# Kernel optimization log

Measured on AMD Instinct MI355X. Metric: run time of the kernel, lower is better.

The kernel has to match this reference:

```python
import jax, jax.numpy as jnp
import numpy as np

IN_C, HEAD_C, EXPAND_C, OUT_C, TIME_C, H = 512, 64, 2048, 512, 256, 8
EPS = 1e-5

def _layernorm(x, g, b):
    mu = jnp.mean(x, axis=-1, keepdims=True)
    var = jnp.mean((x - mu) ** 2, axis=-1, keepdims=True)
    return (x - mu) * jax.lax.rsqrt(var + EPS) * g + b

def setup_inputs() -> dict:
    key = jax.random.key(0)
    ks = jax.random.split(key, 12)
    B, N = 4, 2048
    qkv_dim = HEAD_C * H * 2 + IN_C * H
    def lin(k, fan_in, fan_out):
        bound = 1.0 / np.sqrt(fan_in)
        kw, kb = jax.random.split(k)
        W = jax.random.uniform(kw, (fan_in, fan_out), jnp.float32, -bound, bound)
        b = jax.random.uniform(kb, (fan_out,), jnp.float32, -bound, bound)
        return W, b
    qkv_w, qkv_b = lin(ks[0], IN_C, qkv_dim)
    merge_w, merge_b = lin(ks[1], IN_C * H, IN_C)
    time_w, time_b = lin(ks[2], TIME_C, TIME_C)
    ff1_w, ff1_b = lin(ks[3], IN_C + TIME_C, EXPAND_C)
    ff2_w, ff2_b = lin(ks[4], EXPAND_C, OUT_C)
    return {
        'x': jax.random.normal(ks[5], (B, N, IN_C), jnp.float32),
        't': jax.random.normal(ks[6], (B, TIME_C), jnp.float32),
        'ln1_g': jnp.ones((IN_C,), jnp.float32), 'ln1_b': jnp.zeros((IN_C,), jnp.float32),
        'qkv_w': qkv_w, 'qkv_b': qkv_b,
        'merge_w': merge_w, 'merge_b': merge_b,
        'time_w': time_w, 'time_b': time_b,
        'ln2_g': jnp.ones((IN_C + TIME_C,), jnp.float32), 'ln2_b': jnp.zeros((IN_C + TIME_C,), jnp.float32),
        'ff1_w': ff1_w, 'ff1_b': ff1_b,
        'ff2_w': ff2_w, 'ff2_b': ff2_b,
    }

def reference(x, t, ln1_g, ln1_b, qkv_w, qkv_b, merge_w, merge_b,
              time_w, time_b, ln2_g, ln2_b, ff1_w, ff1_b, ff2_w, ff2_b):
    B, N, _ = x.shape
    scale = HEAD_C ** -0.5
    qkv = _layernorm(x, ln1_g, ln1_b) @ qkv_w + qkv_b
    q, k, v = jnp.split(qkv, [HEAD_C * H, 2 * HEAD_C * H], axis=-1)
    q = q.reshape(B, N, H, HEAD_C)          # B N H Cq
    k = k.reshape(B, N, H, HEAD_C)
    v = v.reshape(B, N, H, IN_C)            # V per head has dim in_c (as in source)
    attn = jnp.einsum('bnhc,bmhc->bhnm', q, k) * scale
    attn = jax.nn.softmax(attn, axis=-1)    # dropout = identity (eval)
    out = jnp.einsum('bhnm,bmhd->bnhd', attn, v).reshape(B, N, H * IN_C)
    x = x + out @ merge_w + merge_b
    tt = (t @ time_w + time_b)[:, None, :]  # B 1 time_c, broadcasts over N
    tt = jnp.broadcast_to(tt, (B, N, TIME_C))
    h = _layernorm(jnp.concatenate([x, tt], axis=-1), ln2_g, ln2_b)
    h = jax.nn.gelu(h @ ff1_w + ff1_b, approximate=False)
    return x + (h @ ff2_w + ff2_b)          # shortcut = Identity (in_c == out_c)
```

## Files before the change

kernel.cpp:

```cpp
#include <hip/hip_runtime.h>

#define IN_C 512
#define HEAD_C 64
#define NHEAD 8
#define TIME_C 256
#define EXPAND_C 2048
#define NB 4
#define NN 2048
#define QKV_DIM 5120
#define ROWS (NB*NN)
#define MERGE_K (NHEAD*IN_C)
#define LN2_C (IN_C+TIME_C)

typedef __bf16 bf16x8 __attribute__((ext_vector_type(8)));
typedef float f32x4 __attribute__((ext_vector_type(4)));
typedef float f32x16 __attribute__((ext_vector_type(16)));
typedef unsigned int u32x4 __attribute__((ext_vector_type(4)));

__device__ __forceinline__ unsigned short f2bf(float f){
  unsigned int u = __builtin_bit_cast(unsigned int, f);
  u += 0x7fffu + ((u >> 16) & 1u);
  return (unsigned short)(u >> 16);
}
__device__ __forceinline__ unsigned int cvtpk(float a, float b){
  unsigned int r;
  asm("v_cvt_pk_bf16_f32 %0, %1, %2" : "=v"(r) : "v"(a), "v"(b));
  return r;
}
__device__ __forceinline__ float vexp2(float x){
  float r;
  asm("v_exp_f32 %0, %1" : "=v"(r) : "v"(x));
  return r;
}
__device__ __forceinline__ float bpermf(float v, int srclane){
  int r = __builtin_amdgcn_ds_bpermute(srclane<<2, __builtin_bit_cast(int, v));
  return __builtin_bit_cast(float, r);
}
__device__ __forceinline__ void gload16(const unsigned short* g, unsigned short* l){
  __builtin_amdgcn_global_load_lds(
      (const __attribute__((address_space(1))) void*)g,
      (__attribute__((address_space(3))) void*)l, 16, 0, 0);
}

__global__ __launch_bounds__(256) void k_transpose_w(const float* __restrict__ W,
                                                     unsigned short* __restrict__ Wt,
                                                     int K, int N){
  __shared__ unsigned short tile[64*72];
  int t = threadIdx.x;
  int kb = blockIdx.y<<6, nb = blockIdx.x<<6;
  {
    int kr = t>>2, nc = (t&3)<<4;
    const float* src = W + (size_t)(kb+kr)*N + nb + nc;
    alignas(16) unsigned short tmp[16];
    #pragma unroll
    for (int j=0;j<16;j+=4){
      float4 v = *(const float4*)(src + j);
      tmp[j+0]=f2bf(v.x); tmp[j+1]=f2bf(v.y); tmp[j+2]=f2bf(v.z); tmp[j+3]=f2bf(v.w);
    }
    *(bf16x8*)&tile[kr*72 + nc]     = *(bf16x8*)&tmp[0];
    *(bf16x8*)&tile[kr*72 + nc + 8] = *(bf16x8*)&tmp[8];
  }
  __syncthreads();
  {
    int nr = t>>2, kc = (t&3)<<4;
    alignas(16) unsigned short ov[16];
    #pragma unroll
    for (int i=0;i<16;i++) ov[i] = tile[(kc+i)*72 + nr];
    unsigned short* dst = Wt + (size_t)(nb+nr)*K + kb + kc;
    *(bf16x8*)dst     = *(bf16x8*)&ov[0];
    *(bf16x8*)(dst+8) = *(bf16x8*)&ov[8];
  }
}

__global__ __launch_bounds__(256) void k_repack_k(const unsigned short* __restrict__ qkv,
                                                  unsigned short* __restrict__ Kf){
  __shared__ unsigned short tile[64*72];
  int j = blockIdx.x;
  int kb64 = j&31, bh = j>>5;
  int b = bh>>3, hh = bh&7;
  int t = threadIdx.x;
  {
    int key = t>>2, sc = t&3;
    const unsigned short* src = qkv + (size_t)(b*NN + kb64*64 + key)*QKV_DIM + IN_C + hh*HEAD_C;
    *(bf16x8*)&tile[key*72 + sc*8]     = *(const bf16x8*)(src + sc*8);
    *(bf16x8*)&tile[key*72 + (sc+4)*8] = *(const bf16x8*)(src + (sc+4)*8);
  }
  __syncthreads();
  int l = t&63, w = t>>6;
  int kb32l = w&1, kk0 = w>>1;
  #pragma unroll
  for (int i=0;i<2;i++){
    int kk = kk0 + i*2;
    alignas(16) unsigned short ov[8];
    #pragma unroll
    for (int jj=0;jj<8;jj++)
      ov[jj] = tile[(kb32l*32 + (l&31))*72 + kk*16 + (l>>5)*8 + jj];
    size_t dst = (((size_t)(bh*64 + kb64*2 + kb32l))*4 + kk)*512 + l*8;
    *(bf16x8*)(Kf + dst) = *(bf16x8*)ov;
  }
}

__global__ __launch_bounds__(256) void k_repack_v(const unsigned short* __restrict__ qkv,
                                                  unsigned short* __restrict__ Vf){
  __shared__ unsigned short tile[64*136];
  int j = blockIdx.x;
  int kb64 = j&31, bh = j>>5;
  int b = bh>>3, hh = bh&7;
  int t = threadIdx.x, l = t&63, w = t>>6;
  int key = t>>2, sc = t&3;
  const unsigned short* srow = qkv + (size_t)(b*NN + kb64*64 + key)*QKV_DIM + 2*IN_C + hh*IN_C;
  for (int p=0;p<4;p++){
    #pragma unroll
    for (int i=0;i<4;i++){
      int ch = sc + i*4;
      *(bf16x8*)&tile[key*136 + ch*8] = *(const bf16x8*)(srow + p*128 + ch*8);
    }
    __syncthreads();
    #pragma unroll
    for (int dbl=0;dbl<4;dbl++){
      alignas(16) unsigned short ov[8];
      #pragma unroll
      for (int jj=0;jj<8;jj++)
        ov[jj] = tile[(w*16 + (l>>5)*8 + jj)*136 + dbl*32 + (l&31)];
      size_t dst = (((size_t)(bh*128 + kb64*4 + w))*16 + p*4 + dbl)*512 + l*8;
      *(bf16x8*)(Vf + dst) = *(bf16x8*)ov;
    }
    __syncthreads();
  }
}

__global__ __launch_bounds__(256) void k_ln1(const float* __restrict__ x,
                                             const float* __restrict__ g,
                                             const float* __restrict__ bta,
                                             unsigned short* __restrict__ out){
  int row = (blockIdx.x<<2) + (threadIdx.x>>6);
  int l = threadIdx.x&63;
  const float* px = x + (size_t)row*IN_C + l*8;
  alignas(16) float v[8];
  *(float4*)&v[0] = *(const float4*)px;
  *(float4*)&v[4] = *(const float4*)(px+4);
  float s=0.f, sq=0.f;
  #pragma unroll
  for (int j=0;j<8;j++){ s+=v[j]; sq+=v[j]*v[j]; }
  #pragma unroll
  for (int d=32; d>0; d>>=1){ s += __shfl_xor(s,d); sq += __shfl_xor(sq,d); }
  float mu = s*(1.f/IN_C);
  float var = sq*(1.f/IN_C) - mu*mu;
  float rstd = rsqrtf(var + 1e-5f);
  alignas(16) unsigned short o[8];
  #pragma unroll
  for (int j=0;j<8;j++){
    int c = l*8+j;
    o[j] = f2bf((v[j]-mu)*rstd*g[c] + bta[c]);
  }
  *(bf16x8*)(out + (size_t)row*IN_C + l*8) = *(bf16x8*)o;
}

__global__ __launch_bounds__(256) void k_time(const float* __restrict__ t,
                                              const float* __restrict__ W,
                                              const float* __restrict__ bias,
                                              float* __restrict__ tt){
  int b = blockIdx.x, j = threadIdx.x;
  float acc = bias[j];
  const float* tr = t + b*TIME_C;
  #pragma unroll 4
  for (int c=0;c<TIME_C;c++) acc = fmaf(tr[c], W[c*TIME_C + j], acc);
  tt[b*TIME_C + j] = acc;
}

__global__ __launch_bounds__(256) void k_ln2(const float* __restrict__ x2,
                                             const float* __restrict__ tt,
                                             const float* __restrict__ g,
                                             const float* __restrict__ bta,
                                             unsigned short* __restrict__ out){
  int row = (blockIdx.x<<2) + (threadIdx.x>>6);
  int l = threadIdx.x&63;
  int bi = row>>11;
  float v[12];
  int c0 = l*12;
  #pragma unroll
  for (int j=0;j<12;j++){
    int c = c0+j;
    v[j] = (c < IN_C) ? x2[(size_t)row*IN_C + c] : tt[bi*TIME_C + c - IN_C];
  }
  float s=0.f, sq=0.f;
  #pragma unroll
  for (int j=0;j<12;j++){ s+=v[j]; sq+=v[j]*v[j]; }
  #pragma unroll
  for (int d=32; d>0; d>>=1){ s += __shfl_xor(s,d); sq += __shfl_xor(sq,d); }
  float mu = s*(1.f/LN2_C);
  float var = sq*(1.f/LN2_C) - mu*mu;
  float rstd = rsqrtf(var + 1e-5f);
  #pragma unroll
  for (int j=0;j<12;j++){
    int c = c0+j;
    out[(size_t)row*LN2_C + c] = f2bf((v[j]-mu)*rstd*g[c] + bta[c]);
  }
}

template<int EPI>
__global__ __launch_bounds__(256) void k_gemm(const unsigned short* __restrict__ A, int lda,
                                              const unsigned short* __restrict__ Bt, int ldb,
                                              const float* __restrict__ bias,
                                              const float* __restrict__ res, int ldres,
                                              void* __restrict__ Cp, int ldc, int K){
  __shared__ unsigned short sA[128*64];
  __shared__ unsigned short sB[128*64];
  int t = threadIdx.x;
  int l = t&63, w = t>>6;
  int m0 = blockIdx.y<<7, n0 = blockIdx.x<<7;
  int wr = (w>>1)<<6, wc = (w&1)<<6;
  int lm = l&15, kq = (l>>4)<<3;
  f32x4 acc[4][4] = {};
  int srow = l>>3, scol = (l&7)<<3;
  const unsigned short* pA = A + (size_t)m0*lda;
  const unsigned short* pB = Bt + (size_t)n0*ldb;
  for (int k0=0; k0<K; k0+=64){
    #pragma unroll
    for (int i=0;i<4;i++){
      int c = w*4 + i;
      gload16(pA + (size_t)(c*8 + srow)*lda + k0 + scol, &sA[c*512]);
      gload16(pB + (size_t)(c*8 + srow)*ldb + k0 + scol, &sB[c*512]);
    }
    __syncthreads();
    bf16x8 af[2][4], bfv[2][4];
    #pragma unroll
    for (int kk=0;kk<2;kk++)
      #pragma unroll
      for (int i=0;i<4;i++){
        af[kk][i]  = *(const bf16x8*)&sA[(wr + i*16 + lm)*64 + kk*32 + kq];
        bfv[kk][i] = *(const bf16x8*)&sB[(wc + i*16 + lm)*64 + kk*32 + kq];
      }
    #pragma unroll
    for (int kk=0;kk<2;kk++)
      #pragma unroll
      for (int mi=0;mi<4;mi++)
        #pragma unroll
        for (int ni=0;ni<4;ni++)
          acc[mi][ni] = __builtin_amdgcn_mfma_f32_16x16x32_bf16(af[kk][mi], bfv[kk][ni], acc[mi][ni], 0,0,0);
    __syncthreads();
  }
  int lr4 = (l>>4)<<2;
  #pragma unroll
  for (int mi=0;mi<4;mi++){
    int row0 = m0 + wr + mi*16 + lr4;
    #pragma unroll
    for (int ni=0;ni<4;ni++){
      int col = n0 + wc + ni*16 + lm;
      float bi = bias[col];
      #pragma unroll
      for (int r=0;r<4;r++){
        float v = acc[mi][ni][r] + bi;
        int row = row0 + r;
        if (EPI==1){
          v += res[(size_t)row*ldres + col];
          ((float*)Cp)[(size_t)row*ldc + col] = v;
        } else if (EPI==2){
          v = 0.5f*v*(1.f + erff(v*0.70710678118f));
          ((unsigned short*)Cp)[(size_t)row*ldc + col] = f2bf(v);
        } else {
          ((unsigned short*)Cp)[(size_t)row*ldc + col] = f2bf(v);
        }
      }
    }
  }
}

__global__ __launch_bounds__(256, 2) void k_attn(const unsigned short* __restrict__ qkv,
                                                 const unsigned short* __restrict__ Kf,
                                                 const unsigned short* __restrict__ Vf,
                                                 unsigned short* __restrict__ out){
  int j = blockIdx.x;
  int xcd = j&7;
  int rest = j>>3;
  int bh = xcd + ((rest>>6)<<3);
  int inner = rest&63;
  int qb = inner>>2, dh = inner&3;
  int b = bh>>3, hh = bh&7;
  int t = threadIdx.x, l = t&63, w = t>>6;
  int q0 = qb*128 + w*32;
  int lq = l&31, half = l>>5;

  bf16x8 qf[4];
  #pragma unroll
  for (int kk=0;kk<4;kk++)
    qf[kk] = *(const bf16x8*)(qkv + (size_t)(b*NN + q0 + lq)*QKV_DIM + hh*HEAD_C + kk*16 + half*8);

  f32x16 o[4] = {};
  float l_ = 0.f;

  const unsigned short* Kbase = Kf + (size_t)bh*64*2048 + l*8;
  const unsigned short* Vbase = Vf + ((size_t)bh*128*16 + dh*4)*512 + l*8;

  auto loadchunk = [&](int c, bf16x8 (&kfv)[4], bf16x8 (&vfv)[2][4]){
    const unsigned short* kp = Kbase + (size_t)c*2048;
    #pragma unroll
    for (int kk=0;kk<4;kk++)
      kfv[kk] = *(const bf16x8*)(kp + kk*512);
    const unsigned short* vp = Vbase + (size_t)c*16384;
    #pragma unroll
    for (int kc=0;kc<2;kc++)
      #pragma unroll
      for (int dn=0;dn<4;dn++)
        vfv[kc][dn] = *(const bf16x8*)(vp + kc*8192 + dn*512);
  };

  auto body = [&](bf16x8 (&kfv)[4], bf16x8 (&vfv)[2][4]){
    f32x16 s = {};
    s = __builtin_amdgcn_mfma_f32_32x32x16_bf16(kfv[0], qf[0], s, 0,0,0);
    s = __builtin_amdgcn_mfma_f32_32x32x16_bf16(kfv[1], qf[1], s, 0,0,0);
    s = __builtin_amdgcn_mfma_f32_32x32x16_bf16(kfv[2], qf[2], s, 0,0,0);
    s = __builtin_amdgcn_mfma_f32_32x32x16_bf16(kfv[3], qf[3], s, 0,0,0);

    float pv[16]; float ps = 0.f;
    #pragma unroll
    for (int r=0;r<16;r++){
      pv[r] = vexp2(s[r]*0.18033688f);
      ps += pv[r];
    }
    ps += __shfl_xor(ps, 32);
    l_ += ps;

    unsigned int wv[8], xw[8];
    #pragma unroll
    for (int jj=0;jj<8;jj++) wv[jj] = cvtpk(pv[2*jj], pv[2*jj+1]);
    #pragma unroll
    for (int jj=0;jj<8;jj++) xw[jj] = __shfl_xor(wv[jj], 32);
    u32x4 f0 = half ? (u32x4){xw[2],xw[3],wv[2],wv[3]} : (u32x4){wv[0],wv[1],xw[0],xw[1]};
    u32x4 f1 = half ? (u32x4){xw[6],xw[7],wv[6],wv[7]} : (u32x4){wv[4],wv[5],xw[4],xw[5]};
    bf16x8 pf0 = __builtin_bit_cast(bf16x8, f0);
    bf16x8 pf1 = __builtin_bit_cast(bf16x8, f1);

    #pragma unroll
    for (int dn=0;dn<4;dn++){
      o[dn] = __builtin_amdgcn_mfma_f32_32x32x16_bf16(pf0, vfv[0][dn], o[dn], 0,0,0);
      o[dn] = __builtin_amdgcn_mfma_f32_32x32x16_bf16(pf1, vfv[1][dn], o[dn], 0,0,0);
    }
  };

  bf16x8 kfa[4], vfa[2][4], kfb[4], vfb[2][4];
  loadchunk(0, kfa, vfa);
  for (int c=0; c<64; c+=2){
    loadchunk(c+1, kfb, vfb);
    body(kfa, vfa);
    if (c+2 < 64) loadchunk(c+2, kfa, vfa);
    body(kfb, vfb);
  }

  float invl = 1.f / l_;
  #pragma unroll
  for (int r=0;r<16;r++){
    int qr = (r&3) + 8*(r>>2) + 4*half;
    float il = bpermf(invl, qr);
    size_t row = (size_t)(b*NN + q0 + qr);
    #pragma unroll
    for (int dn=0;dn<4;dn++){
      int col = hh*IN_C + dh*128 + dn*32 + lq;
      out[row*MERGE_K + col] = f2bf(o[dn][r]*il);
    }
  }
}

extern "C" void kernel_launch(void* const* d_in, const int* in_sizes, int n_in,
                              void* d_out, int out_size, void* d_ws, size_t ws_size,
                              hipStream_t stream){
  const float* x       = (const float*)d_in[0];
  const float* tin     = (const float*)d_in[1];
  const float* ln1_g   = (const float*)d_in[2];
  const float* ln1_b   = (const float*)d_in[3];
  const float* qkv_w   = (const float*)d_in[4];
  const float* qkv_b   = (const float*)d_in[5];
  const float* merge_w = (const float*)d_in[6];
  const float* merge_b = (const float*)d_in[7];
  const float* time_w  = (const float*)d_in[8];
  const float* time_b  = (const float*)d_in[9];
  const float* ln2_g   = (const float*)d_in[10];
  const float* ln2_b   = (const float*)d_in[11];
  const float* ff1_w   = (const float*)d_in[12];
  const float* ff1_b   = (const float*)d_in[13];
  const float* ff2_w   = (const float*)d_in[14];
  const float* ff2_b   = (const float*)d_in[15];

  char* ws = (char*)d_ws;
  size_t off = 0;
  auto alloc = [&](size_t bytes)->void*{ void* p = ws + off; off += (bytes + 255) & ~(size_t)255; return p; };
  unsigned short* wqkvT   = (unsigned short*)alloc((size_t)QKV_DIM*IN_C*2);
  unsigned short* wmergeT = (unsigned short*)alloc((size_t)IN_C*MERGE_K*2);
  unsigned short* wff1T   = (unsigned short*)alloc((size_t)EXPAND_C*LN2_C*2);
  unsigned short* wff2T   = (unsigned short*)alloc((size_t)IN_C*EXPAND_C*2);
  float*          ttb     = (float*)alloc((size_t)NB*TIME_C*4);
  unsigned short* ln1o    = (unsigned short*)alloc((size_t)ROWS*IN_C*2);
  unsigned short* qkvb    = (unsigned short*)alloc((size_t)ROWS*QKV_DIM*2);
  unsigned short* kfrag   = (unsigned short*)alloc((size_t)32*64*4*64*8*2);
  unsigned short* vfrag   = (unsigned short*)alloc((size_t)32*128*16*64*8*2);
  unsigned short* atto    = (unsigned short*)alloc((size_t)ROWS*MERGE_K*2);
  float*          x2      = (float*)alloc((size_t)ROWS*IN_C*4);
  unsigned short* ln2o = vfrag;
  unsigned short* hbuf = qkvb;

  k_transpose_w<<<dim3(QKV_DIM/64, IN_C/64),  256, 0, stream>>>(qkv_w,   wqkvT,   IN_C,     QKV_DIM);
  k_transpose_w<<<dim3(IN_C/64,   MERGE_K/64),256, 0, stream>>>(merge_w, wmergeT, MERGE_K,  IN_C);
  k_transpose_w<<<dim3(EXPAND_C/64, LN2_C/64),256, 0, stream>>>(ff1_w,   wff1T,   LN2_C,    EXPAND_C);
  k_transpose_w<<<dim3(IN_C/64,   EXPAND_C/64),256, 0, stream>>>(ff2_w,  wff2T,   EXPAND_C, IN_C);
  k_time<<<dim3(NB), 256, 0, stream>>>(tin, time_w, time_b, ttb);
  k_ln1<<<dim3(ROWS/4), 256, 0, stream>>>(x, ln1_g, ln1_b, ln1o);

  k_gemm<0><<<dim3(QKV_DIM/128, ROWS/128), 256, 0, stream>>>(ln1o, IN_C, wqkvT, IN_C, qkv_b, nullptr, 0, qkvb, QKV_DIM, IN_C);
  k_repack_k<<<dim3(1024), 256, 0, stream>>>(qkvb, kfrag);
  k_repack_v<<<dim3(1024), 256, 0, stream>>>(qkvb, vfrag);
  k_attn<<<dim3(2048), 256, 0, stream>>>(qkvb, kfrag, vfrag, atto);
  k_gemm<1><<<dim3(IN_C/128, ROWS/128), 256, 0, stream>>>(atto, MERGE_K, wmergeT, MERGE_K, merge_b, x, IN_C, x2, IN_C, MERGE_K);
  k_ln2<<<dim3(ROWS/4), 256, 0, stream>>>(x2, ttb, ln2_g, ln2_b, ln2o);
  k_gemm<2><<<dim3(EXPAND_C/128, ROWS/128), 256, 0, stream>>>(ln2o, LN2_C, wff1T, LN2_C, ff1_b, nullptr, 0, hbuf, EXPAND_C, LN2_C);
  k_gemm<1><<<dim3(IN_C/128, ROWS/128), 256, 0, stream>>>(hbuf, EXPAND_C, wff2T, EXPAND_C, ff2_b, x2, IN_C, (float*)d_out, IN_C, EXPAND_C);

  (void)in_sizes; (void)n_in; (void)out_size; (void)ws_size;
}
```

Baseline: 645.4 us.

## Narrow N-tile for merge/ff2 GEMMs, simplify attention loop, vectorize LN2

Makes the GEMM N tile a template parameter and uses 64-wide tiles for the two GEMMs with output width 512, doubling their block count so the machine is better filled. The attention kernel folds the softmax scale into Q once, drops the per-chunk cross-lane sum in favor of one reduction at the end, and replaces manual double-buffered register prefetch with a simple loop under a higher occupancy bound (4 blocks/SM). LN2 uses float4 loads and 8-byte packed stores. Risks include less latency hiding in attention if the higher occupancy is not reached or causes spills, slight precision change from rounding the pre-scaled Q to bf16, and lower reuse in the narrower GEMM tiles.

```diff
diff --git a/kernel.cpp b/kernel.cpp
--- a/kernel.cpp
+++ b/kernel.cpp
@@ -16,6 +16,7 @@
 typedef float f32x4 __attribute__((ext_vector_type(4)));
 typedef float f32x16 __attribute__((ext_vector_type(16)));
 typedef unsigned int u32x4 __attribute__((ext_vector_type(4)));
+typedef unsigned short u16x4v __attribute__((ext_vector_type(4)));
 
 __device__ __forceinline__ unsigned short f2bf(float f){
   unsigned int u = __builtin_bit_cast(unsigned int, f);
@@ -176,12 +177,15 @@
   int row = (blockIdx.x<<2) + (threadIdx.x>>6);
   int l = threadIdx.x&63;
   int bi = row>>11;
-  float v[12];
   int c0 = l*12;
-  #pragma unroll
-  for (int j=0;j<12;j++){
-    int c = c0+j;
-    v[j] = (c < IN_C) ? x2[(size_t)row*IN_C + c] : tt[bi*TIME_C + c - IN_C];
+  alignas(16) float v[12], gg[12], bb[12];
+  #pragma unroll
+  for (int q=0;q<3;q++){
+    int c = c0 + q*4;
+    const float* src = (c < IN_C) ? &x2[(size_t)row*IN_C + c] : &tt[bi*TIME_C + c - IN_C];
+    *(float4*)&v[q*4]  = *(const float4*)src;
+    *(float4*)&gg[q*4] = *(const float4*)&g[c];
+    *(float4*)&bb[q*4] = *(const float4*)&bta[c];
   }
   float s=0.f, sq=0.f;
   #pragma unroll
@@ -191,27 +195,31 @@
   float mu = s*(1.f/LN2_C);
   float var = sq*(1.f/LN2_C) - mu*mu;
   float rstd = rsqrtf(var + 1e-5f);
-  #pragma unroll
-  for (int j=0;j<12;j++){
-    int c = c0+j;
-    out[(size_t)row*LN2_C + c] = f2bf((v[j]-mu)*rstd*g[c] + bta[c]);
-  }
-}
-
-template<int EPI>
+  alignas(8) unsigned short ov[12];
+  #pragma unroll
+  for (int j=0;j<12;j++)
+    ov[j] = f2bf((v[j]-mu)*rstd*gg[j] + bb[j]);
+  unsigned short* po = out + (size_t)row*LN2_C + c0;
+  *(u16x4v*)&po[0] = *(u16x4v*)&ov[0];
+  *(u16x4v*)&po[4] = *(u16x4v*)&ov[4];
+  *(u16x4v*)&po[8] = *(u16x4v*)&ov[8];
+}
+
+template<int EPI, int BN>
 __global__ __launch_bounds__(256) void k_gemm(const unsigned short* __restrict__ A, int lda,
                                               const unsigned short* __restrict__ Bt, int ldb,
                                               const float* __restrict__ bias,
                                               const float* __restrict__ res, int ldres,
                                               void* __restrict__ Cp, int ldc, int K){
+  constexpr int NI = BN/32;
   __shared__ unsigned short sA[128*64];
-  __shared__ unsigned short sB[128*64];
+  __shared__ unsigned short sB[BN*64];
   int t = threadIdx.x;
   int l = t&63, w = t>>6;
-  int m0 = blockIdx.y<<7, n0 = blockIdx.x<<7;
-  int wr = (w>>1)<<6, wc = (w&1)<<6;
+  int m0 = blockIdx.y<<7, n0 = blockIdx.x*BN;
+  int wr = (w>>1)<<6, wc = (w&1)*(BN/2);
   int lm = l&15, kq = (l>>4)<<3;
-  f32x4 acc[4][4] = {};
+  f32x4 acc[4][NI] = {};
   int srow = l>>3, scol = (l&7)<<3;
   const unsigned short* pA = A + (size_t)m0*lda;
   const unsigned short* pB = Bt + (size_t)n0*ldb;
@@ -220,23 +228,29 @@
     for (int i=0;i<4;i++){
       int c = w*4 + i;
       gload16(pA + (size_t)(c*8 + srow)*lda + k0 + scol, &sA[c*512]);
+    }
+    #pragma unroll
+    for (int i=0;i<BN/32;i++){
+      int c = w*(BN/32) + i;
       gload16(pB + (size_t)(c*8 + srow)*ldb + k0 + scol, &sB[c*512]);
     }
     __syncthreads();
-    bf16x8 af[2][4], bfv[2][4];
-    #pragma unroll
-    for (int kk=0;kk<2;kk++)
+    bf16x8 af[2][4], bfv[2][NI];
+    #pragma unroll
+    for (int kk=0;kk<2;kk++){
       #pragma unroll
-      for (int i=0;i<4;i++){
+      for (int i=0;i<4;i++)
         af[kk][i]  = *(const bf16x8*)&sA[(wr + i*16 + lm)*64 + kk*32 + kq];
+      #pragma unroll
+      for (int i=0;i<NI;i++)
         bfv[kk][i] = *(const bf16x8*)&sB[(wc + i*16 + lm)*64 + kk*32 + kq];
-      }
+    }
     #pragma unroll
     for (int kk=0;kk<2;kk++)
       #pragma unroll
       for (int mi=0;mi<4;mi++)
         #pragma unroll
-        for (int ni=0;ni<4;ni++)
+        for (int ni=0;ni<NI;ni++)
           acc[mi][ni] = __builtin_amdgcn_mfma_f32_16x16x32_bf16(af[kk][mi], bfv[kk][ni], acc[mi][ni], 0,0,0);
     __syncthreads();
   }
@@ -245,7 +259,7 @@
   for (int mi=0;mi<4;mi++){
     int row0 = m0 + wr + mi*16 + lr4;
     #pragma unroll
-    for (int ni=0;ni<4;ni++){
+    for (int ni=0;ni<NI;ni++){
       int col = n0 + wc + ni*16 + lm;
       float bi = bias[col];
       #pragma unroll
@@ -266,7 +280,7 @@
   }
 }
 
-__global__ __launch_bounds__(256, 2) void k_attn(const unsigned short* __restrict__ qkv,
+__global__ __launch_bounds__(256, 4) void k_attn(const unsigned short* __restrict__ qkv,
                                                  const unsigned short* __restrict__ Kf,
                                                  const unsigned short* __restrict__ Vf,
                                                  unsigned short* __restrict__ out){
@@ -283,8 +297,18 @@
 
   bf16x8 qf[4];
   #pragma unroll
-  for (int kk=0;kk<4;kk++)
-    qf[kk] = *(const bf16x8*)(qkv + (size_t)(b*NN + q0 + lq)*QKV_DIM + hh*HEAD_C + kk*16 + half*8);
+  for (int kk=0;kk<4;kk++){
+    bf16x8 raw = *(const bf16x8*)(qkv + (size_t)(b*NN + q0 + lq)*QKV_DIM + hh*HEAD_C + kk*16 + half*8);
+    u32x4 u = __builtin_bit_cast(u32x4, raw);
+    u32x4 rr;
+    #pragma unroll
+    for (int jj=0;jj<4;jj++){
+      float lo = __builtin_bit_cast(float, (u[jj]&0xffffu)<<16);
+      float hi = __builtin_bit_cast(float, u[jj]&0xffff0000u);
+      rr[jj] = cvtpk(lo*0.18033688f, hi*0.18033688f);
+    }
+    qf[kk] = __builtin_bit_cast(bf16x8, rr);
+  }
 
   f32x16 o[4] = {};
   float l_ = 0.f;
@@ -292,33 +316,25 @@
   const unsigned short* Kbase = Kf + (size_t)bh*64*2048 + l*8;
   const unsigned short* Vbase = Vf + ((size_t)bh*128*16 + dh*4)*512 + l*8;
 
-  auto loadchunk = [&](int c, bf16x8 (&kfv)[4], bf16x8 (&vfv)[2][4]){
+  for (int c=0;c<64;c++){
     const unsigned short* kp = Kbase + (size_t)c*2048;
-    #pragma unroll
-    for (int kk=0;kk<4;kk++)
-      kfv[kk] = *(const bf16x8*)(kp + kk*512);
-    const unsigned short* vp = Vbase + (size_t)c*16384;
-    #pragma unroll
-    for (int kc=0;kc<2;kc++)
-      #pragma unroll
-      for (int dn=0;dn<4;dn++)
-        vfv[kc][dn] = *(const bf16x8*)(vp + kc*8192 + dn*512);
-  };
-
-  auto body = [&](bf16x8 (&kfv)[4], bf16x8 (&vfv)[2][4]){
+    bf16x8 kf0 = *(const bf16x8*)(kp);
+    bf16x8 kf1 = *(const bf16x8*)(kp + 512);
+    bf16x8 kf2 = *(const bf16x8*)(kp + 1024);
+    bf16x8 kf3 = *(const bf16x8*)(kp + 1536);
+
     f32x16 s = {};
-    s = __builtin_amdgcn_mfma_f32_32x32x16_bf16(kfv[0], qf[0], s, 0,0,0);
-    s = __builtin_amdgcn_mfma_f32_32x32x16_bf16(kfv[1], qf[1], s, 0,0,0);
-    s = __builtin_amdgcn_mfma_f32_32x32x16_bf16(kfv[2], qf[2], s, 0,0,0);
-    s = __builtin_amdgcn_mfma_f32_32x32x16_bf16(kfv[3], qf[3], s, 0,0,0);
+    s = __builtin_amdgcn_mfma_f32_32x32x16_bf16(kf0, qf[0], s, 0,0,0);
+    s = __builtin_amdgcn_mfma_f32_32x32x16_bf16(kf1, qf[1], s, 0,0,0);
+    s = __builtin_amdgcn_mfma_f32_32x32x16_bf16(kf2, qf[2], s, 0,0,0);
+    s = __builtin_amdgcn_mfma_f32_32x32x16_bf16(kf3, qf[3], s, 0,0,0);
 
     float pv[16]; float ps = 0.f;
     #pragma unroll
     for (int r=0;r<16;r++){
-      pv[r] = vexp2(s[r]*0.18033688f);
+      pv[r] = vexp2(s[r]);
       ps += pv[r];
     }
-    ps += __shfl_xor(ps, 32);
     l_ += ps;
 
     unsigned int wv[8], xw[8];
@@ -331,22 +347,30 @@
     bf16x8 pf0 = __builtin_bit_cast(bf16x8, f0);
     bf16x8 pf1 = __builtin_bit_cast(bf16x8, f1);
 
-    #pragma unroll
-    for (int dn=0;dn<4;dn++){
-      o[dn] = __builtin_amdgcn_mfma_f32_32x32x16_bf16(pf0, vfv[0][dn], o[dn], 0,0,0);
-      o[dn] = __builtin_amdgcn_mfma_f32_32x32x16_bf16(pf1, vfv[1][dn], o[dn], 0,0,0);
-    }
-  };
-
-  bf16x8 kfa[4], vfa[2][4], kfb[4], vfb[2][4];
-  loadchunk(0, kfa, vfa);
-  for (int c=0; c<64; c+=2){
-    loadchunk(c+1, kfb, vfb);
-    body(kfa, vfa);
-    if (c+2 < 64) loadchunk(c+2, kfa, vfa);
-    body(kfb, vfb);
-  }
-
+    const unsigned short* vp = Vbase + (size_t)c*16384;
+    {
+      bf16x8 v0 = *(const bf16x8*)(vp);
+      bf16x8 v1 = *(const bf16x8*)(vp + 512);
+      bf16x8 v2 = *(const bf16x8*)(vp + 1024);
+      bf16x8 v3 = *(const bf16x8*)(vp + 1536);
+      o[0] = __builtin_amdgcn_mfma_f32_32x32x16_bf16(pf0, v0, o[0], 0,0,0);
+      o[1] = __builtin_amdgcn_mfma_f32_32x32x16_bf16(pf0, v1, o[1], 0,0,0);
+      o[2] = __builtin_amdgcn_mfma_f32_32x32x16_bf16(pf0, v2, o[2], 0,0,0);
+      o[3] = __builtin_amdgcn_mfma_f32_32x32x16_bf16(pf0, v3, o[3], 0,0,0);
+    }
+    {
+      bf16x8 v0 = *(const bf16x8*)(vp + 8192);
+      bf16x8 v1 = *(const bf16x8*)(vp + 8704);
+      bf16x8 v2 = *(const bf16x8*)(vp + 9216);
+      bf16x8 v3 = *(const bf16x8*)(vp + 9728);
+      o[0] = __builtin_amdgcn_mfma_f32_32x32x16_bf16(pf1, v0, o[0], 0,0,0);
+      o[1] = __builtin_amdgcn_mfma_f32_32x32x16_bf16(pf1, v1, o[1], 0,0,0);
+      o[2] = __builtin_amdgcn_mfma_f32_32x32x16_bf16(pf1, v2, o[2], 0,0,0);
+      o[3] = __builtin_amdgcn_mfma_f32_32x32x16_bf16(pf1, v3, o[3], 0,0,0);
+    }
+  }
+
+  l_ += __shfl_xor(l_, 32);
   float invl = 1.f / l_;
   #pragma unroll
   for (int r=0;r<16;r++){
@@ -405,14 +429,14 @@
   k_time<<<dim3(NB), 256, 0, stream>>>(tin, time_w, time_b, ttb);
   k_ln1<<<dim3(ROWS/4), 256, 0, stream>>>(x, ln1_g, ln1_b, ln1o);
 
-  k_gemm<0><<<dim3(QKV_DIM/128, ROWS/128), 256, 0, stream>>>(ln1o, IN_C, wqkvT, IN_C, qkv_b, nullptr, 0, qkvb, QKV_DIM, IN_C);
+  k_gemm<0,128><<<dim3(QKV_DIM/128, ROWS/128), 256, 0, stream>>>(ln1o, IN_C, wqkvT, IN_C, qkv_b, nullptr, 0, qkvb, QKV_DIM, IN_C);
   k_repack_k<<<dim3(1024), 256, 0, stream>>>(qkvb, kfrag);
   k_repack_v<<<dim3(1024), 256, 0, stream>>>(qkvb, vfrag);
   k_attn<<<dim3(2048), 256, 0, stream>>>(qkvb, kfrag, vfrag, atto);
-  k_gemm<1><<<dim3(IN_C/128, ROWS/128), 256, 0, stream>>>(atto, MERGE_K, wmergeT, MERGE_K, merge_b, x, IN_C, x2, IN_C, MERGE_K);
+  k_gemm<1,64><<<dim3(IN_C/64, ROWS/128), 256, 0, stream>>>(atto, MERGE_K, wmergeT, MERGE_K, merge_b, x, IN_C, x2, IN_C, MERGE_K);
   k_ln2<<<dim3(ROWS/4), 256, 0, stream>>>(x2, ttb, ln2_g, ln2_b, ln2o);
-  k_gemm<2><<<dim3(EXPAND_C/128, ROWS/128), 256, 0, stream>>>(ln2o, LN2_C, wff1T, LN2_C, ff1_b, nullptr, 0, hbuf, EXPAND_C, LN2_C);
-  k_gemm<1><<<dim3(IN_C/128, ROWS/128), 256, 0, stream>>>(hbuf, EXPAND_C, wff2T, EXPAND_C, ff2_b, x2, IN_C, (float*)d_out, IN_C, EXPAND_C);
+  k_gemm<2,128><<<dim3(EXPAND_C/128, ROWS/128), 256, 0, stream>>>(ln2o, LN2_C, wff1T, LN2_C, ff1_b, nullptr, 0, hbuf, EXPAND_C, LN2_C);
+  k_gemm<1,64><<<dim3(IN_C/64, ROWS/128), 256, 0, stream>>>(hbuf, EXPAND_C, wff2T, EXPAND_C, ff2_b, x2, IN_C, (float*)d_out, IN_C, EXPAND_C);
 
   (void)in_sizes; (void)n_in; (void)out_size; (void)ws_size;
 }
```

New measurement: 624.0 us. -3.3%, faster.
